# Kernel tuning notes

Hardware: AMD Instinct MI355X
Metric: run time of the kernel (lower is better)

Reference implementation:

```python
import jax, jax.numpy as jnp
import numpy as np

ENC_DIM = 256
DEC_DIM = 256
INT_DIM = 256


def setup_inputs() -> dict:
    key = jax.random.key(0)
    k1, k2, k3, k4, k5 = jax.random.split(key, 5)
    B, T = 64, 2048
    encoder_states = jax.random.normal(k1, (B, T, ENC_DIM), dtype=jnp.float32)
    decoder_state = jax.random.normal(k2, (B, DEC_DIM), dtype=jnp.float32)
    s1 = 1.0 / np.sqrt(ENC_DIM)
    s2 = 1.0 / np.sqrt(DEC_DIM)
    s3 = 1.0 / np.sqrt(INT_DIM)
    w1 = jax.random.uniform(k3, (INT_DIM, ENC_DIM), jnp.float32, -s1, s1)
    w2 = jax.random.uniform(k4, (INT_DIM, DEC_DIM), jnp.float32, -s2, s2)
    v = jax.random.uniform(k5, (1, INT_DIM), jnp.float32, -s3, s3)
    return {"encoder_states": encoder_states, "decoder_state": decoder_state,
            "w1": w1, "w2": w2, "v": v}


def reference(encoder_states, decoder_state, w1, w2, v):
    # scores: v @ tanh(W1 e_t + W2 d) for all t at once
    enc_proj = jnp.einsum('bte,ie->bti', encoder_states, w1)      # [B,T,I]
    dec_proj = jnp.einsum('bd,id->bi', decoder_state, w2)          # [B,I]
    scores = jnp.einsum('bti,oi->bt', jnp.tanh(enc_proj + dec_proj[:, None, :]), v)  # [B,T]
    attention_probs = jax.nn.softmax(scores, axis=1)[:, :, None]   # [B,T,1]
    final_context_vec = jnp.sum(attention_probs * encoder_states, axis=1)  # [B,E]
    return final_context_vec, attention_probs
```

## Files before the change

### kernel.cpp

```cpp
#include <hip/hip_runtime.h>
#include <hip/hip_bf16.h>
#include <math.h>

#define Bq 64
#define Tq 2048
#define Eq 256
#define Dq 256
#define Iq 256

using short8  = __attribute__((ext_vector_type(8))) short;
using floatx4 = __attribute__((ext_vector_type(4))) float;

__device__ __forceinline__ float fast_tanh(float x) {
    float e = __expf(2.0f * x);
    return 1.0f - 2.0f / (e + 1.0f);
}

__device__ __forceinline__ ushort f2bf(float x) {
    union { __hip_bfloat16 h; ushort u; } c;
    c.h = __float2bfloat16(x);
    return c.u;
}

__device__ __forceinline__ void async_load16(const void* g, void* l) {
    __builtin_amdgcn_global_load_lds(
        (const __attribute__((address_space(1))) void*)g,
        (__attribute__((address_space(3))) void*)l, 16, 0, 0);
}

__global__ __launch_bounds__(256) void prep_kernel(
    const float* __restrict__ w1, ushort* __restrict__ w1sw,
    const float* __restrict__ dec, const float* __restrict__ w2,
    float* __restrict__ dproj)
{
    if (blockIdx.x < 32) {
        const int kc = blockIdx.x;
        const int i  = threadIdx.x;
        const float* src = w1 + i * Eq + kc * 8;
        float4 f0 = *(const float4*)src;
        float4 f1 = *(const float4*)(src + 4);
        ushort u[8] = { f2bf(f0.x), f2bf(f0.y), f2bf(f0.z), f2bf(f0.w),
                        f2bf(f1.x), f2bf(f1.y), f2bf(f1.z), f2bf(f1.w) };
        *(short8*)&w1sw[(kc * 256 + i) * 8] = *(short8*)u;
    } else {
        const int b = blockIdx.x - 32;
        const int i = threadIdx.x;
        __shared__ float dls[Dq];
        dls[i] = dec[b * Dq + i];
        __syncthreads();
        const float* w2r = w2 + i * Dq;
        float acc = 0.f;
        #pragma unroll 8
        for (int d = 0; d < Dq; ++d) acc += dls[d] * w2r[d];
        dproj[b * Iq + i] = acc;
    }
}

__global__ __launch_bounds__(256) void scores_ctx_kernel(
    const float*  __restrict__ enc,
    const ushort* __restrict__ w1sw,
    const float*  __restrict__ v,
    const float*  __restrict__ dproj,
    float* __restrict__ escore,
    float* __restrict__ ctxp,
    float* __restrict__ denomp)
{
    const int b   = blockIdx.y;
    const int bx  = blockIdx.x;
    const int t0  = bx * 64;
    const int tid = threadIdx.x;
    const int w   = tid >> 6;
    const int l   = tid & 63;
    const int l15 = l & 15;
    const int lq  = l >> 4;

    __shared__ ushort As[64 * 72];
    __shared__ ushort Bs[16384];
    __shared__ float  vls[Iq], dls[Iq];
    __shared__ float  pv[64];

    vls[tid] = v[tid];
    dls[tid] = dproj[b * Iq + tid];

    floatx4 acc[4][4];
    #pragma unroll
    for (int mi = 0; mi < 4; ++mi)
        #pragma unroll
        for (int ni = 0; ni < 4; ++ni)
            acc[mi][ni] = (floatx4)0.f;

    const float* encB = enc + ((size_t)b * Tq + t0) * Eq;

    for (int k0 = 0; k0 < Eq; k0 += 64) {
        const ushort* gb = w1sw + (size_t)(k0 >> 3) * 256 * 8;
        #pragma unroll
        for (int r = 0; r < 8; ++r) {
            const int qbase = r * 256 + w * 64;
            async_load16(gb + (qbase + l) * 8, Bs + qbase * 8);
        }
        #pragma unroll
        for (int r = 0; r < 4; ++r) {
            const int idx = tid + 256 * r;
            const int row = idx >> 4;
            const int c4  = (idx & 15) * 4;
            float4 f = *(const float4*)&encB[row * Eq + k0 + c4];
            ushort4 u;
            u.x = f2bf(f.x); u.y = f2bf(f.y); u.z = f2bf(f.z); u.w = f2bf(f.w);
            *(ushort4*)&As[row * 72 + c4] = u;
        }
        __syncthreads();
        #pragma unroll
        for (int ks = 0; ks < 2; ++ks) {
            const int kloc = ks * 32 + lq * 8;
            short8 af[4], bfv[4];
            #pragma unroll
            for (int mi = 0; mi < 4; ++mi)
                af[mi] = *(const short8*)&As[(mi * 16 + l15) * 72 + kloc];
            #pragma unroll
            for (int ni = 0; ni < 4; ++ni)
                bfv[ni] = *(const short8*)&Bs[((ks * 4 + lq) * 256 + w * 64 + ni * 16 + l15) * 8];
            #pragma unroll
            for (int mi = 0; mi < 4; ++mi)
                #pragma unroll
                for (int ni = 0; ni < 4; ++ni)
                    acc[mi][ni] = __builtin_amdgcn_mfma_f32_16x16x32_bf16(
                        af[mi], bfv[ni], acc[mi][ni], 0, 0, 0);
        }
        __syncthreads();
    }

    float part[4][4];
    #pragma unroll
    for (int mi = 0; mi < 4; ++mi)
        #pragma unroll
        for (int r = 0; r < 4; ++r) part[mi][r] = 0.f;

    #pragma unroll
    for (int ni = 0; ni < 4; ++ni) {
        const int i   = w * 64 + ni * 16 + l15;
        const float vi = vls[i];
        const float dp = dls[i];
        #pragma unroll
        for (int mi = 0; mi < 4; ++mi)
            #pragma unroll
            for (int r = 0; r < 4; ++r)
                part[mi][r] += vi * fast_tanh(acc[mi][ni][r] + dp);
    }

    float* red2 = (float*)Bs;
    #pragma unroll
    for (int mi = 0; mi < 4; ++mi)
        #pragma unroll
        for (int r = 0; r < 4; ++r)
            red2[(w * 64 + mi * 16 + lq * 4 + r) * 20 + l15] = part[mi][r];
    __syncthreads();

    if (tid < 64) {
        float s = 0.f;
        #pragma unroll
        for (int ww = 0; ww < 4; ++ww) {
            const float* rp = red2 + (ww * 64 + tid) * 20;
            float4 q0 = *(const float4*)(rp + 0);
            float4 q1 = *(const float4*)(rp + 4);
            float4 q2 = *(const float4*)(rp + 8);
            float4 q3 = *(const float4*)(rp + 12);
            s += (q0.x + q0.y + q0.z + q0.w) + (q1.x + q1.y + q1.z + q1.w)
               + (q2.x + q2.y + q2.z + q2.w) + (q3.x + q3.y + q3.z + q3.w);
        }
        const float es = __expf(s);
        pv[tid] = es;
        escore[(size_t)b * Tq + t0 + tid] = es;
        float tot = es;
        tot += __shfl_xor(tot, 1);  tot += __shfl_xor(tot, 2);
        tot += __shfl_xor(tot, 4);  tot += __shfl_xor(tot, 8);
        tot += __shfl_xor(tot, 16); tot += __shfl_xor(tot, 32);
        if (tid == 0) denomp[bx * Bq + b] = tot;
    }
    __syncthreads();

    const int tg = tid >> 6;
    const int el = (tid & 63) * 4;
    float4 a = {0.f, 0.f, 0.f, 0.f};
    #pragma unroll 4
    for (int tt = 0; tt < 16; ++tt) {
        const int t = tg * 16 + tt;
        const float pt = pv[t];
        float4 ev = *(const float4*)&encB[t * Eq + el];
        a.x += pt * ev.x; a.y += pt * ev.y; a.z += pt * ev.z; a.w += pt * ev.w;
    }
    float* redf = (float*)As;
    *(float4*)&redf[tg * 256 + el] = a;
    __syncthreads();
    if (tg == 0) {
        float4 a0 = *(const float4*)&redf[0 * 256 + el];
        float4 a1 = *(const float4*)&redf[1 * 256 + el];
        float4 a2 = *(const float4*)&redf[2 * 256 + el];
        float4 a3 = *(const float4*)&redf[3 * 256 + el];
        float4 o;
        o.x = a0.x + a1.x + a2.x + a3.x;
        o.y = a0.y + a1.y + a2.y + a3.y;
        o.z = a0.z + a1.z + a2.z + a3.z;
        o.w = a0.w + a1.w + a2.w + a3.w;
        *(float4*)&ctxp[((size_t)bx * Bq + b) * Eq + el] = o;
    }
}

__global__ __launch_bounds__(256) void finalize_kernel(
    const float* __restrict__ ctxp, const float* __restrict__ denomp,
    float* __restrict__ probs, float* __restrict__ ctx)
{
    const int b   = blockIdx.x;
    const int tid = threadIdx.x;

    float d = denomp[(tid & 31) * Bq + b];
    d += __shfl_xor(d, 1);  d += __shfl_xor(d, 2);  d += __shfl_xor(d, 4);
    d += __shfl_xor(d, 8);  d += __shfl_xor(d, 16);
    const float inv = 1.0f / d;

    float* prow = probs + (size_t)b * Tq + tid * 8;
    float4 p0 = *(const float4*)(prow + 0);
    float4 p1 = *(const float4*)(prow + 4);
    p0.x *= inv; p0.y *= inv; p0.z *= inv; p0.w *= inv;
    p1.x *= inv; p1.y *= inv; p1.z *= inv; p1.w *= inv;
    *(float4*)(prow + 0) = p0;
    *(float4*)(prow + 4) = p1;

    float s = 0.f;
    #pragma unroll 8
    for (int c = 0; c < 32; ++c)
        s += ctxp[((size_t)c * Bq + b) * Eq + tid];
    ctx[b * Eq + tid] = s * inv;
}

extern "C" void kernel_launch(void* const* d_in, const int* in_sizes, int n_in,
                              void* d_out, int out_size, void* d_ws, size_t ws_size,
                              hipStream_t stream) {
    const float* enc = (const float*)d_in[0];
    const float* dec = (const float*)d_in[1];
    const float* w1  = (const float*)d_in[2];
    const float* w2  = (const float*)d_in[3];
    const float* v   = (const float*)d_in[4];

    float* out   = (float*)d_out;
    float* ctx   = out;
    float* probs = out + Bq * Eq;

    char* ws = (char*)d_ws;
    float*  ctxp   = (float*)ws;
    float*  denomp = (float*)(ws + (32*Bq*Eq)*4);
    float*  dproj  = (float*)(ws + (32*Bq*Eq)*4 + 32*Bq*4);
    ushort* w1sw   = (ushort*)(ws + (32*Bq*Eq)*4 + 32*Bq*4 + Bq*Iq*4);

    prep_kernel<<<dim3(96), dim3(256), 0, stream>>>(w1, w1sw, dec, w2, dproj);
    scores_ctx_kernel<<<dim3(Tq / 64, Bq), dim3(256), 0, stream>>>(
        enc, w1sw, v, dproj, probs, ctxp, denomp);
    finalize_kernel<<<dim3(Bq), dim3(256), 0, stream>>>(ctxp, denomp, probs, ctx);
}
```

Baseline: 233.8 us.

## Double-buffer encoder tile, load W1 fragments directly to registers, shuffle-reduce scores

The 32KB LDS staging of W1 is removed; each lane now reads its bf16 W1 fragments straight from global memory (L2-resident) into registers. The encoder A tile is double-buffered in LDS, with the next slice prefetched into registers while MFMAs run, so each k step needs one barrier instead of two. The score reduction across the 16 lanes sharing a row now uses cross-lane shuffles instead of a padded LDS scratch array, and MFMA issue priority is raised. The smaller LDS footprint should let more blocks fit per CU, at the cost of more global load traffic for W1 and higher register pressure.

```diff
diff --git a/kernel.cpp b/kernel.cpp
--- a/kernel.cpp
+++ b/kernel.cpp
@@ -20,12 +20,6 @@
     union { __hip_bfloat16 h; ushort u; } c;
     c.h = __float2bfloat16(x);
     return c.u;
-}
-
-__device__ __forceinline__ void async_load16(const void* g, void* l) {
-    __builtin_amdgcn_global_load_lds(
-        (const __attribute__((address_space(1))) void*)g,
-        (__attribute__((address_space(3))) void*)l, 16, 0, 0);
 }
 
 __global__ __launch_bounds__(256) void prep_kernel(
@@ -74,10 +68,10 @@
     const int l15 = l & 15;
     const int lq  = l >> 4;
 
-    __shared__ ushort As[64 * 72];
-    __shared__ ushort Bs[16384];
-    __shared__ float  vls[Iq], dls[Iq];
-    __shared__ float  pv[64];
+    __shared__ alignas(16) ushort As[2][64 * 72];
+    __shared__ float vls[Iq], dls[Iq];
+    __shared__ float pv[64];
+    __shared__ float swred[4 * 64];
 
     vls[tid] = v[tid];
     dls[tid] = dproj[b * Iq + tid];
@@ -91,42 +85,73 @@
 
     const float* encB = enc + ((size_t)b * Tq + t0) * Eq;
 
-    for (int k0 = 0; k0 < Eq; k0 += 64) {
-        const ushort* gb = w1sw + (size_t)(k0 >> 3) * 256 * 8;
-        #pragma unroll
-        for (int r = 0; r < 8; ++r) {
-            const int qbase = r * 256 + w * 64;
-            async_load16(gb + (qbase + l) * 8, Bs + qbase * 8);
-        }
+    const int srow = tid >> 4;
+    const int sc4  = (tid & 15) * 4;
+
+    {
+        float4 st[4];
+        #pragma unroll
+        for (int r = 0; r < 4; ++r)
+            st[r] = *(const float4*)&encB[(srow + 16 * r) * Eq + sc4];
         #pragma unroll
         for (int r = 0; r < 4; ++r) {
-            const int idx = tid + 256 * r;
-            const int row = idx >> 4;
-            const int c4  = (idx & 15) * 4;
-            float4 f = *(const float4*)&encB[row * Eq + k0 + c4];
             ushort4 u;
-            u.x = f2bf(f.x); u.y = f2bf(f.y); u.z = f2bf(f.z); u.w = f2bf(f.w);
-            *(ushort4*)&As[row * 72 + c4] = u;
-        }
-        __syncthreads();
+            u.x = f2bf(st[r].x); u.y = f2bf(st[r].y);
+            u.z = f2bf(st[r].z); u.w = f2bf(st[r].w);
+            *(ushort4*)&As[0][(srow + 16 * r) * 72 + sc4] = u;
+        }
+    }
+    __syncthreads();
+
+    const ushort* w1b = w1sw + (w * 64 + l15) * 8;
+
+    #pragma unroll
+    for (int k0i = 0; k0i < 4; ++k0i) {
+        const int cur = k0i & 1;
+
+        short8 bfv[2][4];
+        #pragma unroll
+        for (int ks = 0; ks < 2; ++ks) {
+            const int kc = k0i * 8 + ks * 4 + lq;
+            #pragma unroll
+            for (int ni = 0; ni < 4; ++ni)
+                bfv[ks][ni] = *(const short8*)&w1b[((size_t)kc * 256 + ni * 16) * 8];
+        }
+
+        float4 st[4];
+        if (k0i < 3) {
+            #pragma unroll
+            for (int r = 0; r < 4; ++r)
+                st[r] = *(const float4*)&encB[(srow + 16 * r) * Eq + (k0i * 64 + 64) + sc4];
+        }
+
+        __builtin_amdgcn_s_setprio(1);
         #pragma unroll
         for (int ks = 0; ks < 2; ++ks) {
             const int kloc = ks * 32 + lq * 8;
-            short8 af[4], bfv[4];
+            short8 af[4];
             #pragma unroll
             for (int mi = 0; mi < 4; ++mi)
-                af[mi] = *(const short8*)&As[(mi * 16 + l15) * 72 + kloc];
-            #pragma unroll
-            for (int ni = 0; ni < 4; ++ni)
-                bfv[ni] = *(const short8*)&Bs[((ks * 4 + lq) * 256 + w * 64 + ni * 16 + l15) * 8];
+                af[mi] = *(const short8*)&As[cur][(mi * 16 + l15) * 72 + kloc];
             #pragma unroll
             for (int mi = 0; mi < 4; ++mi)
                 #pragma unroll
                 for (int ni = 0; ni < 4; ++ni)
                     acc[mi][ni] = __builtin_amdgcn_mfma_f32_16x16x32_bf16(
-                        af[mi], bfv[ni], acc[mi][ni], 0, 0, 0);
-        }
-        __syncthreads();
+                        af[mi], bfv[ks][ni], acc[mi][ni], 0, 0, 0);
+        }
+        __builtin_amdgcn_s_setprio(0);
+
+        if (k0i < 3) {
+            #pragma unroll
+            for (int r = 0; r < 4; ++r) {
+                ushort4 u;
+                u.x = f2bf(st[r].x); u.y = f2bf(st[r].y);
+                u.z = f2bf(st[r].z); u.w = f2bf(st[r].w);
+                *(ushort4*)&As[cur ^ 1][(srow + 16 * r) * 72 + sc4] = u;
+            }
+            __syncthreads();
+        }
     }
 
     float part[4][4];
@@ -137,7 +162,7 @@
 
     #pragma unroll
     for (int ni = 0; ni < 4; ++ni) {
-        const int i   = w * 64 + ni * 16 + l15;
+        const int i    = w * 64 + ni * 16 + l15;
         const float vi = vls[i];
         const float dp = dls[i];
         #pragma unroll
@@ -147,26 +172,26 @@
                 part[mi][r] += vi * fast_tanh(acc[mi][ni][r] + dp);
     }
 
-    float* red2 = (float*)Bs;
     #pragma unroll
     for (int mi = 0; mi < 4; ++mi)
         #pragma unroll
-        for (int r = 0; r < 4; ++r)
-            red2[(w * 64 + mi * 16 + lq * 4 + r) * 20 + l15] = part[mi][r];
+        for (int r = 0; r < 4; ++r) {
+            float x = part[mi][r];
+            x += __shfl_xor(x, 1); x += __shfl_xor(x, 2);
+            x += __shfl_xor(x, 4); x += __shfl_xor(x, 8);
+            part[mi][r] = x;
+        }
+    if (l15 == 0) {
+        #pragma unroll
+        for (int mi = 0; mi < 4; ++mi)
+            #pragma unroll
+            for (int r = 0; r < 4; ++r)
+                swred[w * 64 + mi * 16 + lq * 4 + r] = part[mi][r];
+    }
     __syncthreads();
 
     if (tid < 64) {
-        float s = 0.f;
-        #pragma unroll
-        for (int ww = 0; ww < 4; ++ww) {
-            const float* rp = red2 + (ww * 64 + tid) * 20;
-            float4 q0 = *(const float4*)(rp + 0);
-            float4 q1 = *(const float4*)(rp + 4);
-            float4 q2 = *(const float4*)(rp + 8);
-            float4 q3 = *(const float4*)(rp + 12);
-            s += (q0.x + q0.y + q0.z + q0.w) + (q1.x + q1.y + q1.z + q1.w)
-               + (q2.x + q2.y + q2.z + q2.w) + (q3.x + q3.y + q3.z + q3.w);
-        }
+        float s = swred[tid] + swred[64 + tid] + swred[128 + tid] + swred[192 + tid];
         const float es = __expf(s);
         pv[tid] = es;
         escore[(size_t)b * Tq + t0 + tid] = es;
@@ -181,14 +206,14 @@
     const int tg = tid >> 6;
     const int el = (tid & 63) * 4;
     float4 a = {0.f, 0.f, 0.f, 0.f};
-    #pragma unroll 4
+    #pragma unroll 8
     for (int tt = 0; tt < 16; ++tt) {
         const int t = tg * 16 + tt;
         const float pt = pv[t];
         float4 ev = *(const float4*)&encB[t * Eq + el];
         a.x += pt * ev.x; a.y += pt * ev.y; a.z += pt * ev.z; a.w += pt * ev.w;
     }
-    float* redf = (float*)As;
+    float* redf = (float*)&As[0][0];
     *(float4*)&redf[tg * 256 + el] = a;
     __syncthreads();
     if (tg == 0) {
```

Result: faster. 224.5 us (-4.0%).
